# Optimization experiments

Measured on AMD Instinct MI355X. Metric: run time of the kernel, lower is better.

The kernel has to match this reference:

```python
import jax, jax.numpy as jnp
import numpy as np

SELU_SCALE = 1.0507009873554805
SELU_ALPHA = 1.6732632423543772

N, C_IN, H, W = 1024, 3, 32, 32
OUT_FEAT, KK, POOL_K = 64, 3, 2
PATCH_DIM = C_IN * KK * KK  # 27


def setup_inputs() -> dict:
    key = jax.random.key(0)
    k1, k2, k3 = jax.random.split(key, 3)
    x = jax.random.normal(k1, (N, C_IN, H, W), dtype=jnp.float32)
    weight = jax.random.normal(k2, (PATCH_DIM, OUT_FEAT), dtype=jnp.float32) * (1.0 / PATCH_DIM ** 0.5)
    bias = jnp.zeros((OUT_FEAT,), dtype=jnp.float32)
    scale_proj = jax.random.normal(k3, (C_IN, OUT_FEAT), dtype=jnp.float32) * 0.1
    scale_bias = jnp.zeros((OUT_FEAT,), dtype=jnp.float32)
    return {"x": x, "weight": weight, "bias": bias,
            "scale_proj": scale_proj, "scale_bias": scale_bias}


def _selu(x):
    return SELU_SCALE * jnp.where(x > 0, x, SELU_ALPHA * jnp.expm1(x))


def reference(x, weight, bias, scale_proj, scale_bias):
    # Unfold ordering is (c, ki, kj) flattened -> weight.T reshapes to OIHW conv kernel.
    w_k = weight.T.reshape(OUT_FEAT, C_IN, KK, KK)
    proj = jax.lax.conv_general_dilated(
        x, w_k, window_strides=(1, 1), padding=[(1, 1), (1, 1)],
        dimension_numbers=("NCHW", "OIHW", "NCHW"))
    proj = proj + bias[None, :, None, None]
    act = _selu(proj)  # (N, 64, H, W)
    # LPPool1d(p=2, k=2, s=2) over flattened (64*H, W): pool along last axis W.
    Wp = W // POOL_K
    a2 = act.reshape(N, OUT_FEAT, H, Wp, POOL_K)
    pooled = jnp.sqrt(jnp.sum(a2 * a2, axis=-1))  # (N, 64, H, Wp)
    channel_summary = x.mean(axis=(2, 3))  # (N, C_in)
    gate = jax.nn.sigmoid(channel_summary @ scale_proj + scale_bias)  # (N, 64)
    out = pooled.mean(axis=(2, 3)) * gate  # (N, 64)
    return out
```

## Files before the change

### kernel.cpp

```cpp
#include <hip/hip_runtime.h>
#include <math.h>

#define SELU_SCALE 1.0507009873554805f
#define SELU_ALPHA 1.6732632423543772f

constexpr int CIN  = 3;
constexpr int HH   = 32;
constexpr int WW   = 32;
constexpr int OUTF = 64;

typedef _Float16 f16x8 __attribute__((ext_vector_type(8)));
typedef _Float16 f16x2 __attribute__((ext_vector_type(2)));
typedef float    f32x4 __attribute__((ext_vector_type(4)));

__device__ __forceinline__ unsigned int pack2(float a, float b) {
    return __builtin_bit_cast(unsigned int, __builtin_amdgcn_cvt_pkrtz(a, b));
}

template <int CTRL, int ROW_MASK>
__device__ __forceinline__ float dpp_add(float v) {
    int sh = __builtin_amdgcn_update_dpp(0, __float_as_int(v),
                                         CTRL, ROW_MASK, 0xf, false);
    return v + __int_as_float(sh);
}
__device__ __forceinline__ float wave64_sum(float v) {
    v = dpp_add<0x111, 0xf>(v);
    v = dpp_add<0x112, 0xf>(v);
    v = dpp_add<0x114, 0xf>(v);
    v = dpp_add<0x118, 0xf>(v);
    v = dpp_add<0x142, 0xa>(v);
    v = dpp_add<0x143, 0xc>(v);
    return v;
}

__device__ __forceinline__ float selu_ns(float s) {
    float e = SELU_ALPHA * (__expf(s) - 1.f);
    return s > 0.f ? s : e;
}

__global__ void pack_weights(const float* __restrict__ weight,
                             const float* __restrict__ bias,
                             uint4* __restrict__ pwB) {
    const int t    = threadIdx.x;
    const int ot   = t >> 6;
    const int lane = t & 63;
    const int oc   = ot * 16 + (lane & 15);
    const int k0   = (lane >> 4) * 8;
    unsigned int d[4];
    #pragma unroll
    for (int r = 0; r < 4; ++r) {
        const int ka = k0 + 2 * r, kb = ka + 1;
        const float wa = (ka < 27) ? weight[ka * OUTF + oc] : (ka == 27 ? bias[oc] : 0.f);
        const float wb = (kb < 27) ? weight[kb * OUTF + oc] : (kb == 27 ? bias[oc] : 0.f);
        d[r] = pack2(wa, wb);
    }
    pwB[ot * 64 + lane] = make_uint4(d[0], d[1], d[2], d[3]);
}

__global__ __launch_bounds__(256, 4) void fused_conv_mfma(
    const float* __restrict__ x,
    const uint4* __restrict__ pwB,
    const float* __restrict__ scale_proj,
    const float* __restrict__ scale_bias,
    float* __restrict__ out)
{
    const int n    = blockIdx.x;
    const int t    = threadIdx.x;
    const int lane = t & 63;
    const int wv   = t >> 6;
    const int quad = lane >> 4;
    const int m16  = lane & 15;

    __shared__ float xs[CIN][34][34];
    __shared__ float red4[4][4][OUTF];
    __shared__ float credu[CIN][4];

    float* xsf = &xs[0][0][0];
    for (int i = t; i < CIN * 34 * 34; i += 256) xsf[i] = 0.f;
    __syncthreads();

    const float* xn = x + (size_t)n * (CIN * HH * WW);
    float cp0 = 0.f, cp1 = 0.f, cp2 = 0.f;
    for (int i = t; i < CIN * HH * WW; i += 256) {
        float v  = xn[i];
        int   c  = i >> 10;
        int   hw = i & 1023;
        xs[c][(hw >> 5) + 1][(hw & 31) + 1] = v;
        if (c == 0) cp0 += v; else if (c == 1) cp1 += v; else cp2 += v;
    }
    cp0 = wave64_sum(cp0);
    cp1 = wave64_sum(cp1);
    cp2 = wave64_sum(cp2);
    if (lane == 63) { credu[0][wv] = cp0; credu[1][wv] = cp1; credu[2][wv] = cp2; }
    __syncthreads();

    f16x8 bfr[4];
    #pragma unroll
    for (int ot = 0; ot < 4; ++ot)
        bfr[ot] = __builtin_bit_cast(f16x8, pwB[ot * 64 + lane]);

    int loff[8];
    #pragma unroll
    for (int j = 0; j < 8; ++j) {
        const int k  = quad * 8 + j;
        const int c  = (k >= 18) ? 2 : (k >= 9 ? 1 : 0);
        const int rm = k - 9 * c;
        const int rr = (rm >= 6) ? 2 : (rm >= 3 ? 1 : 0);
        const int cc = rm - 3 * rr;
        loff[j] = (k < 27) ? (c * 1156 + rr * 34 + cc + m16) : m16;
    }
    const bool g3 = (quad == 3);

    float racc[4] = {0.f, 0.f, 0.f, 0.f};
    const int tile0 = wv * 16;
    const f32x4 zc = {0.f, 0.f, 0.f, 0.f};
    for (int jt = 0; jt < 16; ++jt) {
        const int tile  = tile0 + jt;
        const int sbase = (tile >> 1) * 34 + (tile & 1) * 16;

        float v[8];
        #pragma unroll
        for (int j = 0; j < 8; ++j) v[j] = xsf[sbase + loff[j]];
        v[3] = g3 ? 1.0f : v[3];
        v[4] = g3 ? 0.0f : v[4];
        v[5] = g3 ? 0.0f : v[5];
        v[6] = g3 ? 0.0f : v[6];
        v[7] = g3 ? 0.0f : v[7];

        uint4 au = make_uint4(pack2(v[0], v[1]), pack2(v[2], v[3]),
                              pack2(v[4], v[5]), pack2(v[6], v[7]));
        const f16x8 af = __builtin_bit_cast(f16x8, au);

        #pragma unroll
        for (int ot = 0; ot < 4; ++ot) {
            f32x4 d = __builtin_amdgcn_mfma_f32_16x16x32_f16(af, bfr[ot], zc, 0, 0, 0);
            const float s0 = selu_ns(d[0]);
            const float s1 = selu_ns(d[1]);
            const float s2 = selu_ns(d[2]);
            const float s3 = selu_ns(d[3]);
            racc[ot] += __builtin_amdgcn_sqrtf(fmaf(s0, s0, s1 * s1))
                      + __builtin_amdgcn_sqrtf(fmaf(s2, s2, s3 * s3));
        }
    }

    #pragma unroll
    for (int ot = 0; ot < 4; ++ot)
        red4[wv][quad][ot * 16 + m16] = racc[ot];
    __syncthreads();

    if (t < OUTF) {
        float s = 0.f;
        #pragma unroll
        for (int w = 0; w < 4; ++w)
            #pragma unroll
            for (int q = 0; q < 4; ++q)
                s += red4[w][q][t];
        const float mean = s * (SELU_SCALE / 512.f);
        float g = scale_bias[t];
        #pragma unroll
        for (int c = 0; c < CIN; ++c) {
            const float cs = (credu[c][0] + credu[c][1] + credu[c][2] + credu[c][3])
                             * (1.f / 1024.f);
            g = fmaf(cs, scale_proj[c * OUTF + t], g);
        }
        g = 1.f / (1.f + __expf(-g));
        out[(size_t)n * OUTF + t] = mean * g;
    }
}

extern "C" void kernel_launch(void* const* d_in, const int* in_sizes, int n_in,
                              void* d_out, int out_size, void* d_ws, size_t ws_size,
                              hipStream_t stream) {
    const float* x          = (const float*)d_in[0];
    const float* weight     = (const float*)d_in[1];
    const float* bias       = (const float*)d_in[2];
    const float* scale_proj = (const float*)d_in[3];
    const float* scale_bias = (const float*)d_in[4];
    float* out = (float*)d_out;
    uint4* pwB = (uint4*)d_ws;

    pack_weights<<<1, 256, 0, stream>>>(weight, bias, pwB);
    fused_conv_mfma<<<1024, 256, 0, stream>>>(x, pwB, scale_proj,
                                              scale_bias, out);
}
```

Before: 91.15 us.

## Fuse weight packing into main kernel and fold bias into MFMA accumulator

Removes the separate pack_weights launch. Each block now packs the fp16 weight fragments itself into shared memory, with the global weight reads overlapping the padding zero-fill. The bias is now supplied as the MFMA accumulator input instead of through a ones-column in the A fragment, which removes the per-tile quad-3 selects. The MFMAs are also batched ahead of the SELU work, and the tile loop is unrolled by 2 to improve instruction overlap. In exchange, every block redundantly reads and converts the weights, uses more LDS, and may need more registers.

```diff
diff --git a/kernel.cpp b/kernel.cpp
--- a/kernel.cpp
+++ b/kernel.cpp
@@ -10,7 +10,6 @@
 constexpr int OUTF = 64;
 
 typedef _Float16 f16x8 __attribute__((ext_vector_type(8)));
-typedef _Float16 f16x2 __attribute__((ext_vector_type(2)));
 typedef float    f32x4 __attribute__((ext_vector_type(4)));
 
 __device__ __forceinline__ unsigned int pack2(float a, float b) {
@@ -38,28 +37,10 @@
     return s > 0.f ? s : e;
 }
 
-__global__ void pack_weights(const float* __restrict__ weight,
-                             const float* __restrict__ bias,
-                             uint4* __restrict__ pwB) {
-    const int t    = threadIdx.x;
-    const int ot   = t >> 6;
-    const int lane = t & 63;
-    const int oc   = ot * 16 + (lane & 15);
-    const int k0   = (lane >> 4) * 8;
-    unsigned int d[4];
-    #pragma unroll
-    for (int r = 0; r < 4; ++r) {
-        const int ka = k0 + 2 * r, kb = ka + 1;
-        const float wa = (ka < 27) ? weight[ka * OUTF + oc] : (ka == 27 ? bias[oc] : 0.f);
-        const float wb = (kb < 27) ? weight[kb * OUTF + oc] : (kb == 27 ? bias[oc] : 0.f);
-        d[r] = pack2(wa, wb);
-    }
-    pwB[ot * 64 + lane] = make_uint4(d[0], d[1], d[2], d[3]);
-}
-
 __global__ __launch_bounds__(256, 4) void fused_conv_mfma(
     const float* __restrict__ x,
-    const uint4* __restrict__ pwB,
+    const float* __restrict__ weight,
+    const float* __restrict__ bias,
     const float* __restrict__ scale_proj,
     const float* __restrict__ scale_bias,
     float* __restrict__ out)
@@ -72,11 +53,27 @@
     const int m16  = lane & 15;
 
     __shared__ float xs[CIN][34][34];
+    __shared__ uint4 wfrag[4][64];
     __shared__ float red4[4][4][OUTF];
     __shared__ float credu[CIN][4];
 
     float* xsf = &xs[0][0][0];
     for (int i = t; i < CIN * 34 * 34; i += 256) xsf[i] = 0.f;
+
+    {
+        const int ot = t >> 6, ln = t & 63;
+        const int oc = ot * 16 + (ln & 15);
+        const int k0 = (ln >> 4) * 8;
+        unsigned int d[4];
+        #pragma unroll
+        for (int r = 0; r < 4; ++r) {
+            const int ka = k0 + 2 * r, kb = ka + 1;
+            const float wa = (ka < 27) ? weight[ka * OUTF + oc] : 0.f;
+            const float wb = (kb < 27) ? weight[kb * OUTF + oc] : 0.f;
+            d[r] = pack2(wa, wb);
+        }
+        wfrag[ot][ln] = make_uint4(d[0], d[1], d[2], d[3]);
+    }
     __syncthreads();
 
     const float* xn = x + (size_t)n * (CIN * HH * WW);
@@ -95,9 +92,13 @@
     __syncthreads();
 
     f16x8 bfr[4];
+    f32x4 cb[4];
     #pragma unroll
-    for (int ot = 0; ot < 4; ++ot)
-        bfr[ot] = __builtin_bit_cast(f16x8, pwB[ot * 64 + lane]);
+    for (int ot = 0; ot < 4; ++ot) {
+        bfr[ot] = __builtin_bit_cast(f16x8, wfrag[ot][lane]);
+        const float b = bias[ot * 16 + m16];
+        cb[ot] = (f32x4){b, b, b, b};
+    }
 
     int loff[8];
     #pragma unroll
@@ -109,11 +110,10 @@
         const int cc = rm - 3 * rr;
         loff[j] = (k < 27) ? (c * 1156 + rr * 34 + cc + m16) : m16;
     }
-    const bool g3 = (quad == 3);
 
     float racc[4] = {0.f, 0.f, 0.f, 0.f};
     const int tile0 = wv * 16;
-    const f32x4 zc = {0.f, 0.f, 0.f, 0.f};
+    #pragma unroll 2
     for (int jt = 0; jt < 16; ++jt) {
         const int tile  = tile0 + jt;
         const int sbase = (tile >> 1) * 34 + (tile & 1) * 16;
@@ -121,25 +121,28 @@
         float v[8];
         #pragma unroll
         for (int j = 0; j < 8; ++j) v[j] = xsf[sbase + loff[j]];
-        v[3] = g3 ? 1.0f : v[3];
-        v[4] = g3 ? 0.0f : v[4];
-        v[5] = g3 ? 0.0f : v[5];
-        v[6] = g3 ? 0.0f : v[6];
-        v[7] = g3 ? 0.0f : v[7];
 
         uint4 au = make_uint4(pack2(v[0], v[1]), pack2(v[2], v[3]),
                               pack2(v[4], v[5]), pack2(v[6], v[7]));
         const f16x8 af = __builtin_bit_cast(f16x8, au);
 
+        f32x4 dd[4];
+        #pragma unroll
+        for (int ot = 0; ot < 4; ++ot)
+            dd[ot] = __builtin_amdgcn_mfma_f32_16x16x32_f16(af, bfr[ot], cb[ot], 0, 0, 0);
+
+        float s[16];
         #pragma unroll
         for (int ot = 0; ot < 4; ++ot) {
-            f32x4 d = __builtin_amdgcn_mfma_f32_16x16x32_f16(af, bfr[ot], zc, 0, 0, 0);
-            const float s0 = selu_ns(d[0]);
-            const float s1 = selu_ns(d[1]);
-            const float s2 = selu_ns(d[2]);
-            const float s3 = selu_ns(d[3]);
-            racc[ot] += __builtin_amdgcn_sqrtf(fmaf(s0, s0, s1 * s1))
-                      + __builtin_amdgcn_sqrtf(fmaf(s2, s2, s3 * s3));
+            s[4 * ot + 0] = selu_ns(dd[ot][0]);
+            s[4 * ot + 1] = selu_ns(dd[ot][1]);
+            s[4 * ot + 2] = selu_ns(dd[ot][2]);
+            s[4 * ot + 3] = selu_ns(dd[ot][3]);
+        }
+        #pragma unroll
+        for (int ot = 0; ot < 4; ++ot) {
+            racc[ot] += __builtin_amdgcn_sqrtf(fmaf(s[4*ot+0], s[4*ot+0], s[4*ot+1] * s[4*ot+1]))
+                      + __builtin_amdgcn_sqrtf(fmaf(s[4*ot+2], s[4*ot+2], s[4*ot+3] * s[4*ot+3]));
         }
     }
 
@@ -177,9 +180,7 @@
     const float* scale_proj = (const float*)d_in[3];
     const float* scale_bias = (const float*)d_in[4];
     float* out = (float*)d_out;
-    uint4* pwB = (uint4*)d_ws;
 
-    pack_weights<<<1, 256, 0, stream>>>(weight, bias, pwB);
-    fused_conv_mfma<<<1024, 256, 0, stream>>>(x, pwB, scale_proj,
-                                              scale_bias, out);
+    fused_conv_mfma<<<1024, 256, 0, stream>>>(x, weight, bias,
+                                              scale_proj, scale_bias, out);
 }
```

New measurement: 88.75 us. -2.6%, faster.

## Split each image across two blocks and finish the gate in a second kernel

Applied to the files above, without the earlier changes.

Each image is now processed by two blocks, each covering 16 rows with a halo, which doubles the grid to 2048 blocks and roughly halves per-block shared memory. The launch bound is raised to allow more resident blocks. Weight packing moves from its own kernel into every conv block's shared memory. Per-half partial sums and channel sums go to a workspace, and a small second kernel combines them and applies the sigmoid gate. The cost is an extra kernel launch plus redundant weight packing and halo loads in every block.

```diff
diff --git a/kernel.cpp b/kernel.cpp
--- a/kernel.cpp
+++ b/kernel.cpp
@@ -8,9 +8,12 @@
 constexpr int HH   = 32;
 constexpr int WW   = 32;
 constexpr int OUTF = 64;
+constexpr int XSH  = 18;
+constexpr int XSW  = 34;
+constexpr int XSC  = XSH * XSW;
+constexpr int PSTRIDE = 68;
 
 typedef _Float16 f16x8 __attribute__((ext_vector_type(8)));
-typedef _Float16 f16x2 __attribute__((ext_vector_type(2)));
 typedef float    f32x4 __attribute__((ext_vector_type(4)));
 
 __device__ __forceinline__ unsigned int pack2(float a, float b) {
@@ -38,55 +41,56 @@
     return s > 0.f ? s : e;
 }
 
-__global__ void pack_weights(const float* __restrict__ weight,
-                             const float* __restrict__ bias,
-                             uint4* __restrict__ pwB) {
-    const int t    = threadIdx.x;
-    const int ot   = t >> 6;
-    const int lane = t & 63;
-    const int oc   = ot * 16 + (lane & 15);
-    const int k0   = (lane >> 4) * 8;
-    unsigned int d[4];
-    #pragma unroll
-    for (int r = 0; r < 4; ++r) {
-        const int ka = k0 + 2 * r, kb = ka + 1;
-        const float wa = (ka < 27) ? weight[ka * OUTF + oc] : (ka == 27 ? bias[oc] : 0.f);
-        const float wb = (kb < 27) ? weight[kb * OUTF + oc] : (kb == 27 ? bias[oc] : 0.f);
-        d[r] = pack2(wa, wb);
-    }
-    pwB[ot * 64 + lane] = make_uint4(d[0], d[1], d[2], d[3]);
-}
-
-__global__ __launch_bounds__(256, 4) void fused_conv_mfma(
+__global__ __launch_bounds__(256, 8) void conv_half(
     const float* __restrict__ x,
-    const uint4* __restrict__ pwB,
-    const float* __restrict__ scale_proj,
-    const float* __restrict__ scale_bias,
-    float* __restrict__ out)
+    const float* __restrict__ weight,
+    const float* __restrict__ bias,
+    float* __restrict__ part)
 {
-    const int n    = blockIdx.x;
+    const int b    = blockIdx.x;
+    const int n    = b >> 1;
+    const int h0   = (b & 1) << 4;
     const int t    = threadIdx.x;
     const int lane = t & 63;
     const int wv   = t >> 6;
     const int quad = lane >> 4;
     const int m16  = lane & 15;
 
-    __shared__ float xs[CIN][34][34];
+    __shared__ float xs[CIN * XSC];
+    __shared__ uint4 wfrag[4][64];
     __shared__ float red4[4][4][OUTF];
     __shared__ float credu[CIN][4];
 
-    float* xsf = &xs[0][0][0];
-    for (int i = t; i < CIN * 34 * 34; i += 256) xsf[i] = 0.f;
+    for (int i = t; i < CIN * XSC; i += 256) xs[i] = 0.f;
+    {
+        const int ot = t >> 6, ln = t & 63;
+        const int oc = ot * 16 + (ln & 15);
+        const int k0 = (ln >> 4) * 8;
+        unsigned int d[4];
+        #pragma unroll
+        for (int r = 0; r < 4; ++r) {
+            const int ka = k0 + 2 * r, kb = ka + 1;
+            const float wa = (ka < 27) ? weight[ka * OUTF + oc]
+                                       : (ka == 27 ? bias[oc] : 0.f);
+            const float wb = (kb < 27) ? weight[kb * OUTF + oc]
+                                       : (kb == 27 ? bias[oc] : 0.f);
+            d[r] = pack2(wa, wb);
+        }
+        wfrag[ot][ln] = make_uint4(d[0], d[1], d[2], d[3]);
+    }
     __syncthreads();
 
     const float* xn = x + (size_t)n * (CIN * HH * WW);
     float cp0 = 0.f, cp1 = 0.f, cp2 = 0.f;
-    for (int i = t; i < CIN * HH * WW; i += 256) {
-        float v  = xn[i];
-        int   c  = i >> 10;
-        int   hw = i & 1023;
-        xs[c][(hw >> 5) + 1][(hw & 31) + 1] = v;
-        if (c == 0) cp0 += v; else if (c == 1) cp1 += v; else cp2 += v;
+    for (int i = t; i < CIN * XSH * WW; i += 256) {
+        const int c   = i / 576;
+        const int rc  = i - c * 576;
+        const int row = rc >> 5, col = rc & 31;
+        const int gr  = h0 - 1 + row;
+        const float v = (gr >= 0 && gr < HH) ? xn[c * 1024 + gr * 32 + col] : 0.f;
+        xs[c * XSC + row * XSW + col + 1] = v;
+        const float vo = (row >= 1 && row <= 16) ? v : 0.f;
+        if (c == 0) cp0 += vo; else if (c == 1) cp1 += vo; else cp2 += vo;
     }
     cp0 = wave64_sum(cp0);
     cp1 = wave64_sum(cp1);
@@ -97,7 +101,7 @@
     f16x8 bfr[4];
     #pragma unroll
     for (int ot = 0; ot < 4; ++ot)
-        bfr[ot] = __builtin_bit_cast(f16x8, pwB[ot * 64 + lane]);
+        bfr[ot] = __builtin_bit_cast(f16x8, wfrag[ot][lane]);
 
     int loff[8];
     #pragma unroll
@@ -107,28 +111,28 @@
         const int rm = k - 9 * c;
         const int rr = (rm >= 6) ? 2 : (rm >= 3 ? 1 : 0);
         const int cc = rm - 3 * rr;
-        loff[j] = (k < 27) ? (c * 1156 + rr * 34 + cc + m16) : m16;
+        loff[j] = (k < 27) ? (c * XSC + rr * XSW + cc + m16) : m16;
     }
     const bool g3 = (quad == 3);
 
     float racc[4] = {0.f, 0.f, 0.f, 0.f};
-    const int tile0 = wv * 16;
     const f32x4 zc = {0.f, 0.f, 0.f, 0.f};
-    for (int jt = 0; jt < 16; ++jt) {
-        const int tile  = tile0 + jt;
-        const int sbase = (tile >> 1) * 34 + (tile & 1) * 16;
+    #pragma unroll 1
+    for (int jt = 0; jt < 8; ++jt) {
+        const int tile  = wv * 8 + jt;
+        const int sbase = (tile >> 1) * XSW + (tile & 1) * 16;
 
         float v[8];
         #pragma unroll
-        for (int j = 0; j < 8; ++j) v[j] = xsf[sbase + loff[j]];
+        for (int j = 0; j < 8; ++j) v[j] = xs[sbase + loff[j]];
         v[3] = g3 ? 1.0f : v[3];
         v[4] = g3 ? 0.0f : v[4];
         v[5] = g3 ? 0.0f : v[5];
         v[6] = g3 ? 0.0f : v[6];
         v[7] = g3 ? 0.0f : v[7];
 
-        uint4 au = make_uint4(pack2(v[0], v[1]), pack2(v[2], v[3]),
-                              pack2(v[4], v[5]), pack2(v[6], v[7]));
+        const uint4 au = make_uint4(pack2(v[0], v[1]), pack2(v[2], v[3]),
+                                    pack2(v[4], v[5]), pack2(v[6], v[7]));
         const f16x8 af = __builtin_bit_cast(f16x8, au);
 
         #pragma unroll
@@ -148,6 +152,7 @@
         red4[wv][quad][ot * 16 + m16] = racc[ot];
     __syncthreads();
 
+    float* pb = part + (size_t)b * PSTRIDE;
     if (t < OUTF) {
         float s = 0.f;
         #pragma unroll
@@ -155,17 +160,35 @@
             #pragma unroll
             for (int q = 0; q < 4; ++q)
                 s += red4[w][q][t];
-        const float mean = s * (SELU_SCALE / 512.f);
-        float g = scale_bias[t];
-        #pragma unroll
-        for (int c = 0; c < CIN; ++c) {
-            const float cs = (credu[c][0] + credu[c][1] + credu[c][2] + credu[c][3])
-                             * (1.f / 1024.f);
-            g = fmaf(cs, scale_proj[c * OUTF + t], g);
-        }
-        g = 1.f / (1.f + __expf(-g));
-        out[(size_t)n * OUTF + t] = mean * g;
-    }
+        pb[t] = s;
+    } else if (t < OUTF + CIN) {
+        const int c = t - OUTF;
+        pb[t] = credu[c][0] + credu[c][1] + credu[c][2] + credu[c][3];
+    }
+}
+
+__global__ __launch_bounds__(256, 4) void gate_store(
+    const float* __restrict__ part,
+    const float* __restrict__ scale_proj,
+    const float* __restrict__ scale_bias,
+    float* __restrict__ out)
+{
+    const int gid = blockIdx.x * 256 + threadIdx.x;
+    const int n   = gid >> 6;
+    const int oc  = gid & 63;
+    const float* p0 = part + (size_t)(2 * n) * PSTRIDE;
+    const float* p1 = p0 + PSTRIDE;
+
+    const float s    = p0[oc] + p1[oc];
+    const float mean = s * (SELU_SCALE / 512.f);
+    float g = scale_bias[oc];
+    #pragma unroll
+    for (int c = 0; c < CIN; ++c) {
+        const float cs = (p0[OUTF + c] + p1[OUTF + c]) * (1.f / 1024.f);
+        g = fmaf(cs, scale_proj[c * OUTF + oc], g);
+    }
+    g = 1.f / (1.f + __expf(-g));
+    out[gid] = mean * g;
 }
 
 extern "C" void kernel_launch(void* const* d_in, const int* in_sizes, int n_in,
@@ -176,10 +199,9 @@
     const float* bias       = (const float*)d_in[2];
     const float* scale_proj = (const float*)d_in[3];
     const float* scale_bias = (const float*)d_in[4];
-    float* out = (float*)d_out;
-    uint4* pwB = (uint4*)d_ws;
-
-    pack_weights<<<1, 256, 0, stream>>>(weight, bias, pwB);
-    fused_conv_mfma<<<1024, 256, 0, stream>>>(x, pwB, scale_proj,
-                                              scale_bias, out);
-}
+    float* out  = (float*)d_out;
+    float* part = (float*)d_ws;
+
+    conv_half<<<2048, 256, 0, stream>>>(x, weight, bias, part);
+    gate_store<<<256, 256, 0, stream>>>(part, scale_proj, scale_bias, out);
+}
```

New measurement: 90.41 us. Within noise of the previous version (-0.8%).
